# Kernel optimization log

Measured on AMD Instinct MI355X. Metric: run time of the kernel, lower is better.

Reference implementation:

```python
import jax, jax.numpy as jnp
import numpy as np

PI = float(np.pi)


def _conv2d(x, w, b, pad):
    out = jax.lax.conv_general_dilated(x, w, (1, 1), ((pad, pad), (pad, pad)),
                                       dimension_numbers=('NCHW', 'OIHW', 'NCHW'))
    return out + b[None, :, None, None]


def _group_norm(x, gamma, beta, groups, eps=1e-5):
    B, C, h, w = x.shape
    xg = x.reshape(B, groups, C // groups, h, w)
    mu = xg.mean(axis=(2, 3, 4), keepdims=True)
    var = xg.var(axis=(2, 3, 4), keepdims=True)
    xn = ((xg - mu) / jnp.sqrt(var + eps)).reshape(B, C, h, w)
    return xn * gamma[None, :, None, None] + beta[None, :, None, None]


def _l2n(x, eps=1e-12):
    return x / jnp.maximum(jnp.linalg.norm(x, axis=1, keepdims=True), eps)


def _dense_sift(x):
    # kornia DenseSIFTDescriptor defaults: 8 ang bins, 4x4 spatial bins,
    # spatial_bin_size=4, rootsift=True, clipval=0.2, stride=1, padding=1
    eps = 1e-10
    NA = 8
    # 'diff' spatial gradient with replicate padding, normalized (/2)
    xp = jnp.pad(x, ((0, 0), (0, 0), (1, 1), (1, 1)), mode='edge')
    gx = (xp[:, :, 1:-1, 2:] - xp[:, :, 1:-1, :-2]) * 0.5
    gy = (xp[:, :, 2:, 1:-1] - xp[:, :, :-2, 1:-1]) * 0.5
    mag = jnp.sqrt(gx * gx + gy * gy + eps)[:, 0]           # [B,H,W]
    ori = jnp.arctan2(gy, gx + eps)[:, 0] + 2.0 * PI
    o_big = NA * ori / (2.0 * PI)
    bo0f = jnp.floor(o_big)
    wo1_ = o_big - bo0f
    wo0 = (1.0 - wo1_) * mag
    wo1 = wo1_ * mag
    bo0 = bo0f.astype(jnp.int32) % NA
    bo1 = (bo0 + 1) % NA
    bins = jnp.arange(NA).reshape(1, NA, 1, 1)
    ang = ((bo0[:, None] == bins).astype(x.dtype) * wo0[:, None]
           + (bo1[:, None] == bins).astype(x.dtype) * wo1[:, None])  # [B,8,H,W]
    # SIFT pooling kernel ksize=4 (triangle weights), conv pad=2 -> H+1,W+1
    xc2 = np.array([0.5, 1.5, 1.5, 0.5], np.float32)
    pool1 = np.outer(xc2, xc2) / 4.0
    pk = jnp.asarray(np.tile(pool1[None, None], (NA, 1, 1, 1)))  # depthwise [8,1,4,4]
    pooled = jax.lax.conv_general_dilated(ang, pk, (1, 1), ((2, 2), (2, 2)),
                dimension_numbers=('NCHW', 'OIHW', 'NCHW'), feature_group_count=NA)
    # identity reshape conv: 128 = 8 ang * 4*4 spatial bins, pad=1 -> back to H,W
    rk = jnp.asarray(np.eye(128, dtype=np.float32).reshape(128, NA, 4, 4))
    out = jax.lax.conv_general_dilated(pooled, rk, (1, 1), ((1, 1), (1, 1)),
                dimension_numbers=('NCHW', 'OIHW', 'NCHW'))
    out = jnp.clip(_l2n(out), 0.0, 0.2)
    out = _l2n(out)
    l1 = jnp.maximum(jnp.sum(jnp.abs(out), axis=1, keepdims=True), 1e-12)
    return jnp.sqrt(out / l1 + eps)  # rootsift


def _joint_bilateral(x, guide, ksize=5, sigma_color=0.1, sigma_space=1.5):
    pad = ksize // 2
    ax = np.arange(ksize, dtype=np.float32) - ksize // 2
    g1 = np.exp(-ax ** 2 / (2.0 * sigma_space ** 2))
    g1 = g1 / g1.sum()
    sk = np.outer(g1, g1)  # normalized 5x5 gaussian space kernel
    xp = jnp.pad(x, ((0, 0), (0, 0), (pad, pad), (pad, pad)), mode='reflect')
    gp = jnp.pad(guide, ((0, 0), (0, 0), (pad, pad), (pad, pad)), mode='reflect')
    h, w = x.shape[2], x.shape[3]
    inv = -0.5 / (sigma_color ** 2)
    num = jnp.zeros_like(x)
    den = jnp.zeros((x.shape[0], 1, h, w), x.dtype)
    for dy in range(ksize):           # fixed 5x5 tap loop, accumulated in-place
        for dx in range(ksize):
            gs = gp[:, :, dy:dy + h, dx:dx + w]
            cd = jnp.sum(jnp.abs(gs - guide), axis=1, keepdims=True) ** 2  # l1 squared
            wgt = sk[dy, dx] * jnp.exp(inv * cd)
            num = num + wgt * xp[:, :, dy:dy + h, dx:dx + w]
            den = den + wgt
    return num / den


def _forward(x, gt, w1, b1, g1w, g1b, w2, b2, g2w, g2b, w3, b3, g3w, g3b,
             w4, b4, g4w, g4b, w5, b5):
    orig = x
    f = _dense_sift(x)
    f = jax.nn.relu(_group_norm(_conv2d(f, w1, b1, 2), g1w, g1b, 8))
    f = jax.nn.relu(_group_norm(_conv2d(f, w2, b2, 1), g2w, g2b, 8))
    f = jax.nn.relu(_group_norm(_conv2d(f, w3, b3, 1), g3w, g3b, 4))
    f = jax.nn.relu(_group_norm(_conv2d(f, w4, b4, 1), g4w, g4b, 4))
    f = _conv2d(f, w5, b5, 1)
    # rgb_to_yuv(gt)[:, 1:] as guidance
    r, g, b = gt[:, 0], gt[:, 1], gt[:, 2]
    u = -0.147 * r - 0.289 * g + 0.436 * b
    v = 0.615 * r - 0.515 * g - 0.100 * b
    guide = jnp.stack([u, v], axis=1)
    f = _joint_bilateral(f, guide)

    def _rescale(c, lo, hi):
        c = (c - c.min()) / (c.max() - c.min() + 1e-6)  # global min/max over B,H,W
        c = jnp.clip(c, 0.0, 1.0)
        return c * (hi - lo) + lo

    U = _rescale(f[:, 0], -0.436, 0.436)
    V = _rescale(f[:, 1], -0.615, 0.615)
    Y = orig[:, 0]
    R = Y + 1.14 * V
    G = Y - 0.396 * U - 0.581 * V
    B = Y + 2.029 * U
    return jnp.stack([R, G, B], axis=1)


def setup_inputs() -> dict:
    key = jax.random.key(0)
    ks = jax.random.split(key, 16)
    B = 4
    d = {
        'x': jax.random.uniform(ks[0], (B, 1, 270, 512), jnp.float32),
        'gt': jax.random.uniform(ks[1], (B, 3, 270, 512), jnp.float32),
        'w1': jax.random.normal(ks[2], (64, 128, 5, 5), jnp.float32) * 0.02,
        'b1': jnp.zeros((64,), jnp.float32),
        'g1w': jnp.ones((64,), jnp.float32), 'g1b': jnp.zeros((64,), jnp.float32),
        'w2': jax.random.normal(ks[3], (32, 64, 3, 3), jnp.float32) * 0.04,
        'b2': jnp.zeros((32,), jnp.float32),
        'g2w': jnp.ones((32,), jnp.float32), 'g2b': jnp.zeros((32,), jnp.float32),
        'w3': jax.random.normal(ks[4], (16, 32, 3, 3), jnp.float32) * 0.05,
        'b3': jnp.zeros((16,), jnp.float32),
        'g3w': jnp.ones((16,), jnp.float32), 'g3b': jnp.zeros((16,), jnp.float32),
        'w4': jax.random.normal(ks[5], (8, 16, 3, 3), jnp.float32) * 0.08,
        'b4': jnp.zeros((8,), jnp.float32),
        'g4w': jnp.ones((8,), jnp.float32), 'g4b': jnp.zeros((8,), jnp.float32),
        'w5': jax.random.normal(ks[6], (2, 8, 3, 3), jnp.float32) * 0.1,
        'b5': jnp.zeros((2,), jnp.float32),
    }
    return d


def reference(x, gt, w1, b1, g1w, g1b, w2, b2, g2w, g2b, w3, b3, g3w, g3b,
              w4, b4, g4w, g4b, w5, b5):
    return _forward(x, gt, w1, b1, g1w, g1b, w2, b2, g2w, g2b, w3, b3, g3w, g3b,
                    w4, b4, g4w, g4b, w5, b5)
```

## Files before the change

### kernel.cpp

```cpp
#include <hip/hip_runtime.h>

constexpr int NB  = 4;
constexpr int IH  = 270;
constexpr int IW  = 512;
constexpr int NPIX = IH * IW;
constexpr int PH  = 271;
constexpr int PW  = 513;
constexpr float TWO_PI_F = 6.28318530717958647692f;

typedef short  bf16x8 __attribute__((ext_vector_type(8)));
typedef float floatx4 __attribute__((ext_vector_type(4)));

__device__ inline unsigned short f2bf(float x) {
  union { float f; unsigned u; } un; un.f = x;
  unsigned r = un.u + 0x7fff + ((un.u >> 16) & 1);
  return (unsigned short)(r >> 16);
}
__device__ inline float bf2f(unsigned short u) {
  union { unsigned u; float f; } x; x.u = ((unsigned)u) << 16; return x.f;
}
__device__ inline unsigned fkey(float f) {
  unsigned u = __float_as_uint(f);
  return (u & 0x80000000u) ? ~u : (u | 0x80000000u);
}
__device__ inline float funkey(unsigned k) {
  unsigned u = (k & 0x80000000u) ? (k ^ 0x80000000u) : ~k;
  return __uint_as_float(u);
}
__device__ inline void gn_coef_thread(const float* __restrict__ stats,
                                      const float* __restrict__ gamma,
                                      const float* __restrict__ beta,
                                      float* cA, float* cB, int C, int chper, int b) {
  int c = threadIdx.x;
  if (c < C) {
    int g0 = (c / chper) * chper;
    float S = 0.f, S2 = 0.f;
    for (int k = 0; k < chper; k++) {
      S  += stats[(b * C + g0 + k) * 2];
      S2 += stats[(b * C + g0 + k) * 2 + 1];
    }
    double Nd = (double)chper * NPIX;
    double mu = (double)S / Nd;
    double var = (double)S2 / Nd - mu * mu;
    double rstd = 1.0 / sqrt(var + 1e-5);
    float A = (float)rstd * gamma[c];
    cA[c] = A;
    cB[c] = beta[c] - (float)mu * A;
  }
}

__device__ inline void mfma_pack_one(const float* __restrict__ w, short* __restrict__ wB,
                                     int i, int CO, int CI, int KK, int CHUNKS) {
  int j = i & 7, l = (i >> 3) & 63, f = i >> 9;
  int t = f % KK; int fc = f / KK; int cc = fc % CHUNKS; int g = fc / CHUNKS;
  int ci = cc * 32 + ((l >> 4) << 3) + j;
  int co = g * 16 + (l & 15);
  float v = (ci < CI && co < CO) ? w[((size_t)co * CI + ci) * KK + t] : 0.f;
  wB[i] = (short)f2bf(v);
}
__device__ inline void repack_one(const float* __restrict__ w, float* __restrict__ wT,
                                  int i, int CO, int CI, int KK) {
  int o = i / (CI * KK);
  int r = i % (CI * KK);
  int ci = r / KK, kk = r % KK;
  wT[(kk * CI + ci) * CO + o] = w[i];
}
__global__ __launch_bounds__(256) void prep_kernel(
    const float* __restrict__ w1, const float* __restrict__ w2,
    const float* __restrict__ w3, const float* __restrict__ w4,
    const float* __restrict__ w5,
    short* __restrict__ w1B, short* __restrict__ w2B, short* __restrict__ w3B,
    float* __restrict__ w4T, float* __restrict__ w5T) {
  constexpr int N1 = 4 * 4 * 25 * 512;
  constexpr int N2 = 2 * 2 * 9 * 512;
  constexpr int N3 = 1 * 1 * 9 * 512;
  constexpr int N4 = 8 * 16 * 9;
  constexpr int N5 = 2 * 8 * 9;
  int i = blockIdx.x * 256 + threadIdx.x;
  if (i < N1) { mfma_pack_one(w1, w1B, i, 64, 128, 25, 4); return; }
  i -= N1;
  if (i < N2) { mfma_pack_one(w2, w2B, i, 32, 64, 9, 2); return; }
  i -= N2;
  if (i < N3) { mfma_pack_one(w3, w3B, i, 16, 32, 9, 1); return; }
  i -= N3;
  if (i < N4) { repack_one(w4, w4T, i, 8, 16, 9); return; }
  i -= N4;
  if (i < N5) { repack_one(w5, w5T, i, 2, 8, 9); return; }
}

__global__ __launch_bounds__(256) void sift_desc_kernel(
    const float* __restrict__ x, short* __restrict__ descg) {
  const int b = blockIdx.z;
  const int x0 = blockIdx.x * 16, y0 = blockIdx.y * 16;
  __shared__ float xs[24][25];
  __shared__ float wo0[22][23], wo1[22][23];
  __shared__ int   bo0[22][23];
  __shared__ float pooled[8][19][20];
  __shared__ float s1s[256], gs[256];
  const int tid = threadIdx.x;
  const float* xb = x + (size_t)b * NPIX;

  for (int t = tid; t < 576; t += 256) {
    int r = t / 24, c = t % 24;
    int gy = min(max(y0 - 4 + r, 0), IH - 1);
    int gx = min(max(x0 - 4 + c, 0), IW - 1);
    xs[r][c] = xb[gy * IW + gx];
  }
  __syncthreads();

  for (int t = tid; t < 484; t += 256) {
    int r = t / 22, c = t % 22;
    int gy = y0 - 3 + r, gx = x0 - 3 + c;
    float w0 = 0.f, w1v = 0.f; int b0 = 0;
    if (gy >= 0 && gy < IH && gx >= 0 && gx < IW) {
      float gxv = (xs[r + 1][c + 2] - xs[r + 1][c]) * 0.5f;
      float gyv = (xs[r + 2][c + 1] - xs[r][c + 1]) * 0.5f;
      float mag = sqrtf(gxv * gxv + gyv * gyv + 1e-10f);
      float ori = atan2f(gyv, gxv + 1e-10f) + TWO_PI_F;
      float obig = ori * (8.0f / TWO_PI_F);
      float bf = floorf(obig);
      float w1_ = obig - bf;
      w0  = (1.0f - w1_) * mag;
      w1v = w1_ * mag;
      b0  = ((int)bf) & 7;
    }
    wo0[r][c] = w0; wo1[r][c] = w1v; bo0[r][c] = b0;
  }
  __syncthreads();

  const float pwt[4] = {0.25f, 0.75f, 0.75f, 0.25f};
  for (int t = tid; t < 361; t += 256) {
    int pr = t / 19, pc = t % 19;
    int py = y0 - 1 + pr, px = x0 - 1 + pc;
    float acc[8] = {0, 0, 0, 0, 0, 0, 0, 0};
    if (py >= 0 && py < PH && px >= 0 && px < PW) {
      #pragma unroll
      for (int i = 0; i < 4; i++) {
        #pragma unroll
        for (int j = 0; j < 4; j++) {
          float w0 = wo0[pr + i][pc + j], w1v = wo1[pr + i][pc + j];
          int b0 = bo0[pr + i][pc + j];
          int b1i = (b0 + 1) & 7;
          float pw = pwt[i] * pwt[j];
          #pragma unroll
          for (int a = 0; a < 8; a++) {
            float add = (a == b0 ? w0 : 0.f) + (a == b1i ? w1v : 0.f);
            acc[a] = fmaf(pw, add, acc[a]);
          }
        }
      }
    }
    #pragma unroll
    for (int a = 0; a < 8; a++) pooled[a][pr][pc] = acc[a];
  }
  __syncthreads();

  {
    int py = tid >> 4, px = tid & 15;
    int y = y0 + py;
    float s1 = 0.f, g = 0.f;
    if (y < IH) {
      float sum2 = 0.f;
      for (int c = 0; c < 128; c++) {
        int a = c >> 4, i = (c >> 2) & 3, j = c & 3;
        float p = pooled[a][py + i][px + j];
        sum2 = fmaf(p, p, sum2);
      }
      s1 = 1.0f / fmaxf(sqrtf(sum2), 1e-12f);
      float st2 = 0.f, st = 0.f;
      for (int c = 0; c < 128; c++) {
        int a = c >> 4, i = (c >> 2) & 3, j = c & 3;
        float p = pooled[a][py + i][px + j];
        float tv = fminf(p * s1, 0.2f);
        st2 = fmaf(tv, tv, st2);
        st += tv;
      }
      float s2 = 1.0f / fmaxf(sqrtf(st2), 1e-12f);
      float l1 = fmaxf(s2 * st, 1e-12f);
      g = s2 / l1;
    }
    s1s[tid] = s1; gs[tid] = g;
  }
  __syncthreads();

  for (int k = 0; k < 16; k++) {
    int gidx = k * 256 + tid;
    int cc = gidx >> 10, pix = (gidx >> 2) & 255, sub = gidx & 3;
    int py = pix >> 4, px = pix & 15;
    int y = y0 + py;
    if (y >= IH) continue;
    float s1v = s1s[pix], gv = gs[pix];
    int a = cc * 2 + (sub >> 1);
    unsigned short v8[8];
    #pragma unroll
    for (int jj = 0; jj < 8; jj++) {
      int i = (sub * 2 + (jj >> 2)) & 3;
      int j = jj & 3;
      float p = pooled[a][py + i][px + j];
      v8[jj] = f2bf(sqrtf(fminf(p * s1v, 0.2f) * gv + 1e-10f));
    }
    uint4 pk;
    pk.x = (unsigned)v8[0] | ((unsigned)v8[1] << 16);
    pk.y = (unsigned)v8[2] | ((unsigned)v8[3] << 16);
    pk.z = (unsigned)v8[4] | ((unsigned)v8[5] << 16);
    pk.w = (unsigned)v8[6] | ((unsigned)v8[7] << 16);
    size_t base = ((size_t)(b * 4 + cc) * NPIX + (size_t)y * IW + (x0 + px)) * 32 + sub * 8;
    *(uint4*)(descg + base) = pk;
  }
}

__global__ __launch_bounds__(256, 2) void conv1_mfma_kernel(
    const short* __restrict__ descg, const short* __restrict__ w1B,
    const float* __restrict__ bias, unsigned short* __restrict__ out,
    float* __restrict__ stats) {
  const int b = blockIdx.z;
  const int x0 = blockIdx.x * 16, y0 = blockIdx.y * 16;
  __shared__ __align__(16) char smem_raw[33408];
  short* desc = (short*)smem_raw;
  float* cout = (float*)smem_raw;

  const int tid = threadIdx.x;
  const int wave = tid >> 6, lane = tid & 63;
  const int quad = lane >> 4, lm = lane & 15;

  floatx4 acc[4][4];
  #pragma unroll
  for (int n = 0; n < 4; n++)
    #pragma unroll
    for (int i = 0; i < 4; i++) acc[n][i] = (floatx4){0.f, 0.f, 0.f, 0.f};

  for (int cc = 0; cc < 4; cc++) {
    __syncthreads();
    const short* dg = descg + (size_t)(b * 4 + cc) * NPIX * 32;
    for (int u = tid; u < 1600; u += 256) {
      int pos = u >> 2, sub = u & 3;
      int r = pos / 20, c = pos % 20;
      int gy = y0 - 2 + r, gx = x0 - 2 + c;
      uint4 val = {0u, 0u, 0u, 0u};
      if (gy >= 0 && gy < IH && gx >= 0 && gx < IW)
        val = *(const uint4*)(dg + ((size_t)gy * IW + gx) * 32 + sub * 8);
      *(uint4*)(desc + pos * 40 + sub * 8) = val;
    }
    __syncthreads();

    #pragma unroll
    for (int ky = 0; ky < 5; ky++) {
      #pragma unroll
      for (int kx = 0; kx < 5; kx++) {
        bf16x8 bfr[4];
        #pragma unroll
        for (int n = 0; n < 4; n++) {
          int f = (n * 4 + cc) * 25 + ky * 5 + kx;
          bfr[n] = *(const bf16x8*)(w1B + ((size_t)f << 9) + (lane << 3));
        }
        bf16x8 av[4];
        #pragma unroll
        for (int i = 0; i < 4; i++) {
          int mt = wave * 4 + i;
          av[i] = *(const bf16x8*)(desc + ((mt + ky) * 20 + lm + kx) * 40 + quad * 8);
        }
        #pragma unroll
        for (int n = 0; n < 4; n++)
          #pragma unroll
          for (int i = 0; i < 4; i++)
            acc[n][i] = __builtin_amdgcn_mfma_f32_16x16x32_bf16(av[i], bfr[n], acc[n][i], 0, 0, 0);
      }
    }
  }

  unsigned short* ob = out + (size_t)b * 64 * NPIX;
  for (int h = 0; h < 2; h++) {
    __syncthreads();
    #pragma unroll
    for (int nn = 0; nn < 2; nn++)
      #pragma unroll
      for (int i = 0; i < 4; i++)
        #pragma unroll
        for (int r = 0; r < 4; r++)
          cout[(nn * 16 + lm) * 261 + (wave * 4 + i) * 16 + quad * 4 + r] = acc[h * 2 + nn][i][r];
    __syncthreads();
    for (int v = tid; v < 8192; v += 256) {
      int col = v >> 8, px = v & 255;
      int y = y0 + (px >> 4), x = x0 + (px & 15);
      if (y < IH)
        ob[(size_t)(h * 32 + col) * NPIX + y * IW + x] = f2bf(cout[col * 261 + px] + bias[h * 32 + col]);
    }
    int col = tid >> 3, seg = tid & 7;
    int co = h * 32 + col;
    float bv = bias[co];
    float sum = 0.f, sq = 0.f;
    #pragma unroll
    for (int rr = 0; rr < 2; rr++) {
      int row = seg * 2 + rr;
      if (y0 + row < IH) {
        #pragma unroll
        for (int k = 0; k < 16; k++) {
          float vv = cout[col * 261 + row * 16 + k] + bv;
          sum += vv; sq += vv * vv;
        }
      }
    }
    sum += __shfl_down(sum, 4); sq += __shfl_down(sq, 4);
    sum += __shfl_down(sum, 2); sq += __shfl_down(sq, 2);
    sum += __shfl_down(sum, 1); sq += __shfl_down(sq, 1);
    if ((tid & 7) == 0) {
      atomicAdd(&stats[(b * 64 + co) * 2], sum);
      atomicAdd(&stats[(b * 64 + co) * 2 + 1], sq);
    }
  }
}

template <int CI, int CO, int CHPER, bool STATS>
__global__ __launch_bounds__(256) void convk3_mfma_kernel(
    const unsigned short* __restrict__ xin, const short* __restrict__ wB,
    const float* __restrict__ bias, const float* __restrict__ statsIn,
    const float* __restrict__ gamma, const float* __restrict__ beta,
    float* __restrict__ statsOut, unsigned short* __restrict__ out) {
  constexpr int CHUNKS = CI / 32;
  constexpr int G = CO / 16;
  constexpr int MPW = 2 * G;
  constexpr int CIS = CI + 8;
  constexpr int TILE_B = 180 * CIS * 2;
  constexpr int COUT_B = CO * 133 * 4;
  constexpr int UNION_B = TILE_B > COUT_B ? TILE_B : COUT_B;
  __shared__ __align__(16) char sm[UNION_B + CI * 8];
  short* tile = (short*)sm;
  float* cout = (float*)sm;
  float* cA = (float*)(sm + UNION_B);
  float* cB = cA + CI;

  const int b = blockIdx.z;
  const int x0 = blockIdx.x * 16, y0 = blockIdx.y * 8;
  const int tid = threadIdx.x;
  const int wave = tid >> 6, lane = tid & 63;
  const int quad = lane >> 4, lm = lane & 15;
  const int n = wave % G, mh = wave / G;

  gn_coef_thread(statsIn, gamma, beta, cA, cB, CI, CHPER, b);
  __syncthreads();

  const unsigned short* xb = xin + (size_t)b * CI * NPIX;
  for (int v = tid; v < (CI / 2) * 180; v += 256) {
    int cp = v / 180, pos = v % 180;
    int r = pos / 18, c = pos % 18;
    int gy = y0 - 1 + r, gx = x0 - 1 + c;
    float v0 = 0.f, v1 = 0.f;
    if (gy >= 0 && gy < IH && gx >= 0 && gx < IW) {
      v0 = fmaxf(fmaf(bf2f(xb[(size_t)(2 * cp) * NPIX + gy * IW + gx]), cA[2 * cp], cB[2 * cp]), 0.f);
      v1 = fmaxf(fmaf(bf2f(xb[(size_t)(2 * cp + 1) * NPIX + gy * IW + gx]), cA[2 * cp + 1], cB[2 * cp + 1]), 0.f);
    }
    unsigned pk = (unsigned)f2bf(v0) | ((unsigned)f2bf(v1) << 16);
    *(unsigned*)(tile + pos * CIS + 2 * cp) = pk;
  }
  __syncthreads();

  floatx4 acc[MPW];
  #pragma unroll
  for (int i = 0; i < MPW; i++) acc[i] = (floatx4){0.f, 0.f, 0.f, 0.f};

  #pragma unroll
  for (int cc = 0; cc < CHUNKS; cc++) {
    #pragma unroll
    for (int ky = 0; ky < 3; ky++) {
      #pragma unroll
      for (int kx = 0; kx < 3; kx++) {
        int f = (n * CHUNKS + cc) * 9 + ky * 3 + kx;
        bf16x8 bfr = *(const bf16x8*)(wB + ((size_t)f << 9) + (lane << 3));
        #pragma unroll
        for (int i = 0; i < MPW; i++) {
          int mt = mh * MPW + i;
          bf16x8 av = *(const bf16x8*)(tile + ((mt + ky) * 18 + lm + kx) * CIS + cc * 32 + quad * 8);
          acc[i] = __builtin_amdgcn_mfma_f32_16x16x32_bf16(av, bfr, acc[i], 0, 0, 0);
        }
      }
    }
  }
  __syncthreads();
  #pragma unroll
  for (int i = 0; i < MPW; i++) {
    #pragma unroll
    for (int r = 0; r < 4; r++) {
      int pixel = (mh * MPW + i) * 16 + quad * 4 + r;
      cout[(n * 16 + lm) * 133 + pixel] = acc[i][r];
    }
  }
  __syncthreads();
  unsigned short* ob = out + (size_t)b * CO * NPIX;
  for (int v = tid; v < CO * 128; v += 256) {
    int co = v >> 7, px = v & 127;
    int y = y0 + (px >> 4), x = x0 + (px & 15);
    if (y < IH) ob[(size_t)co * NPIX + y * IW + x] = f2bf(cout[co * 133 + px] + bias[co]);
  }
  if (STATS) {
    constexpr int TPC = 256 / CO;
    constexpr int PXT = 128 / TPC;
    int col = tid / TPC, seg = tid % TPC;
    float bv = bias[col];
    float sum = 0.f, sq = 0.f;
    #pragma unroll
    for (int k = 0; k < PXT; k++) {
      int p = seg * PXT + k;
      if (y0 + (p >> 4) < IH) {
        float vv = cout[col * 133 + p] + bv;
        sum += vv; sq += vv * vv;
      }
    }
    #pragma unroll
    for (int off = TPC / 2; off > 0; off >>= 1) {
      sum += __shfl_down(sum, off);
      sq  += __shfl_down(sq, off);
    }
    if (seg == 0) {
      atomicAdd(&statsOut[(b * CO + col) * 2], sum);
      atomicAdd(&statsOut[(b * CO + col) * 2 + 1], sq);
    }
  }
}

template <int CI, int CO, int CHPER, bool STATS, bool OUT_BF16>
__global__ __launch_bounds__(256) void convs_kernel(
    const unsigned short* __restrict__ xin, const float* __restrict__ wT,
    const float* __restrict__ bias, const float* __restrict__ statsIn,
    const float* __restrict__ gamma, const float* __restrict__ beta,
    float* __restrict__ statsOut, void* __restrict__ outv) {
  constexpr int OPT = CO / 2;
  const int b = blockIdx.z;
  const int x0 = blockIdx.x * 16, y0 = blockIdx.y * 8;
  __shared__ float tile[CI * 180];
  __shared__ float cA[CI], cB[CI];
  __shared__ float ssum[CO], ssq[CO];
  gn_coef_thread(statsIn, gamma, beta, cA, cB, CI, CHPER, b);
  if (STATS && threadIdx.x < CO) { ssum[threadIdx.x] = 0.f; ssq[threadIdx.x] = 0.f; }
  __syncthreads();
  const unsigned short* xb = xin + (size_t)b * CI * NPIX;
  for (int t = threadIdx.x; t < CI * 180; t += 256) {
    int ci = t / 180, rc = t % 180, r = rc / 18, c = rc % 18;
    int gy = y0 - 1 + r, gx = x0 - 1 + c;
    float v = 0.f;
    if (gy >= 0 && gy < IH && gx >= 0 && gx < IW)
      v = fmaxf(fmaf(bf2f(xb[(size_t)ci * NPIX + gy * IW + gx]), cA[ci], cB[ci]), 0.f);
    tile[t] = v;
  }
  __syncthreads();
  const int t = threadIdx.x;
  const int px = t & 127, og = t >> 7;
  const int pyy = px >> 4, pxx = px & 15;
  const int oc0 = og * OPT;
  const int y = y0 + pyy, x = x0 + pxx;
  float acc[OPT] = {};
  for (int ky = 0; ky < 3; ky++) {
    for (int kx = 0; kx < 3; kx++) {
      const float* wrow = wT + (size_t)((ky * 3 + kx) * CI) * CO + oc0;
      for (int ci = 0; ci < CI; ci++) {
        float v = tile[ci * 180 + (pyy + ky) * 18 + pxx + kx];
        #pragma unroll
        for (int o = 0; o < OPT; o++) acc[o] = fmaf(v, wrow[ci * CO + o], acc[o]);
      }
    }
  }
  if (y < IH) {
    #pragma unroll
    for (int o = 0; o < OPT; o++) {
      float vv = acc[o] + bias[oc0 + o];
      if (OUT_BF16) {
        unsigned short* ob = (unsigned short*)outv + (size_t)b * CO * NPIX;
        ob[(size_t)(oc0 + o) * NPIX + y * IW + x] = f2bf(vv);
      } else {
        float* ob = (float*)outv + (size_t)b * CO * NPIX;
        ob[(size_t)(oc0 + o) * NPIX + y * IW + x] = vv;
      }
      if (STATS) {
        atomicAdd(&ssum[oc0 + o], vv);
        atomicAdd(&ssq[oc0 + o], vv * vv);
      }
    }
  }
  if (STATS) {
    __syncthreads();
    if (threadIdx.x < CO) {
      atomicAdd(&statsOut[(b * CO + threadIdx.x) * 2], ssum[threadIdx.x]);
      atomicAdd(&statsOut[(b * CO + threadIdx.x) * 2 + 1], ssq[threadIdx.x]);
    }
  }
}

__global__ __launch_bounds__(256) void bilateral_kernel(
    const float* __restrict__ f, const float* __restrict__ gt,
    float* __restrict__ out, unsigned* __restrict__ mmbits) {
  const int b = blockIdx.z;
  const int x0 = blockIdx.x * 16, y0 = blockIdx.y * 16;
  __shared__ float gu[20][20], gv[20][20], f0s[20][20], f1s[20][20];
  __shared__ float red[4][4];
  const float* gtb = gt + (size_t)b * 3 * NPIX;
  const float* fb = f + (size_t)b * 2 * NPIX;
  for (int t = threadIdx.x; t < 400; t += 256) {
    int r = t / 20, c = t % 20;
    int gy = y0 - 2 + r, gx = x0 - 2 + c;
    if (gy < 0) gy = -gy;
    if (gy > IH - 1) gy = 2 * (IH - 1) - gy;
    if (gx < 0) gx = -gx;
    if (gx > IW - 1) gx = 2 * (IW - 1) - gx;
    int p = gy * IW + gx;
    float rr = gtb[p], gg = gtb[NPIX + p], bb = gtb[2 * NPIX + p];
    gu[r][c]  = -0.147f * rr - 0.289f * gg + 0.436f * bb;
    gv[r][c]  =  0.615f * rr - 0.515f * gg - 0.100f * bb;
    f0s[r][c] = fb[p];
    f1s[r][c] = fb[NPIX + p];
  }
  __syncthreads();
  const int t = threadIdx.x;
  const int lx = t % 16, ly = t / 16;
  const int y = y0 + ly, x = x0 + lx;
  const bool valid = (y < IH);

  float o0 = 0.f, o1 = 0.f;
  if (valid) {
    float g1v[5];
    float s = 0.f;
    #pragma unroll
    for (int k = 0; k < 5; k++) {
      float a = (float)(k - 2);
      g1v[k] = expf(-a * a / 4.5f);
      s += g1v[k];
    }
    #pragma unroll
    for (int k = 0; k < 5; k++) g1v[k] /= s;
    float cu = gu[ly + 2][lx + 2], cv = gv[ly + 2][lx + 2];
    float num0 = 0.f, num1 = 0.f, den = 0.f;
    #pragma unroll
    for (int dy = 0; dy < 5; dy++) {
      #pragma unroll
      for (int dx = 0; dx < 5; dx++) {
        float du = fabsf(gu[ly + dy][lx + dx] - cu) + fabsf(gv[ly + dy][lx + dx] - cv);
        float wgt = g1v[dy] * g1v[dx] * expf(-50.0f * du * du);
        num0 = fmaf(wgt, f0s[ly + dy][lx + dx], num0);
        num1 = fmaf(wgt, f1s[ly + dy][lx + dx], num1);
        den += wgt;
      }
    }
    o0 = num0 / den; o1 = num1 / den;
    float* ob = out + (size_t)b * 2 * NPIX;
    ob[y * IW + x] = o0;
    ob[NPIX + y * IW + x] = o1;
  }
  float mn0 = valid ? o0 : 1e30f,  mx0 = valid ? o0 : -1e30f;
  float mn1 = valid ? o1 : 1e30f,  mx1 = valid ? o1 : -1e30f;
  #pragma unroll
  for (int off = 32; off > 0; off >>= 1) {
    mn0 = fminf(mn0, __shfl_xor(mn0, off));
    mx0 = fmaxf(mx0, __shfl_xor(mx0, off));
    mn1 = fminf(mn1, __shfl_xor(mn1, off));
    mx1 = fmaxf(mx1, __shfl_xor(mx1, off));
  }
  if ((t & 63) == 0) {
    red[t >> 6][0] = mn0; red[t >> 6][1] = mx0;
    red[t >> 6][2] = mn1; red[t >> 6][3] = mx1;
  }
  __syncthreads();
  if (t == 0) {
    for (int w = 1; w < 4; w++) {
      red[0][0] = fminf(red[0][0], red[w][0]);
      red[0][1] = fmaxf(red[0][1], red[w][1]);
      red[0][2] = fminf(red[0][2], red[w][2]);
      red[0][3] = fmaxf(red[0][3], red[w][3]);
    }
    atomicMax(&mmbits[0], fkey(red[0][1]));
    atomicMax(&mmbits[1], fkey(red[0][3]));
    atomicMin(&mmbits[2], fkey(red[0][0]));
    atomicMin(&mmbits[3], fkey(red[0][2]));
  }
}

__global__ __launch_bounds__(256) void final_kernel(
    const float* __restrict__ bil, const float* __restrict__ x,
    const unsigned* __restrict__ mmbits, float* __restrict__ out) {
  int i = blockIdx.x * 256 + threadIdx.x;
  if (i >= NB * NPIX) return;
  float mx0 = funkey(mmbits[0]), mx1 = funkey(mmbits[1]);
  float mn0 = funkey(mmbits[2]), mn1 = funkey(mmbits[3]);
  int b = i / NPIX, p = i % NPIX;
  float f0 = bil[(size_t)b * 2 * NPIX + p];
  float f1 = bil[(size_t)b * 2 * NPIX + NPIX + p];
  float U = (f0 - mn0) / (mx0 - mn0 + 1e-6f);
  U = fminf(fmaxf(U, 0.f), 1.f) * 0.872f - 0.436f;
  float V = (f1 - mn1) / (mx1 - mn1 + 1e-6f);
  V = fminf(fmaxf(V, 0.f), 1.f) * 1.23f - 0.615f;
  float Y = x[(size_t)b * NPIX + p];
  float* ob = out + (size_t)b * 3 * NPIX;
  ob[p]            = Y + 1.14f * V;
  ob[NPIX + p]     = Y - 0.396f * U - 0.581f * V;
  ob[2 * NPIX + p] = Y + 2.029f * U;
}

extern "C" void kernel_launch(void* const* d_in, const int* in_sizes, int n_in,
                              void* d_out, int out_size, void* d_ws, size_t ws_size,
                              hipStream_t stream) {
  const float* x   = (const float*)d_in[0];
  const float* gt  = (const float*)d_in[1];
  const float* w1  = (const float*)d_in[2];
  const float* b1  = (const float*)d_in[3];
  const float* g1w = (const float*)d_in[4];
  const float* g1b = (const float*)d_in[5];
  const float* w2  = (const float*)d_in[6];
  const float* b2  = (const float*)d_in[7];
  const float* g2w = (const float*)d_in[8];
  const float* g2b = (const float*)d_in[9];
  const float* w3  = (const float*)d_in[10];
  const float* b3  = (const float*)d_in[11];
  const float* g3w = (const float*)d_in[12];
  const float* g3b = (const float*)d_in[13];
  const float* w4  = (const float*)d_in[14];
  const float* b4  = (const float*)d_in[15];
  const float* g4w = (const float*)d_in[16];
  const float* g4b = (const float*)d_in[17];
  const float* w5  = (const float*)d_in[18];
  const float* b5  = (const float*)d_in[19];
  float* out = (float*)d_out;

  char* ws = (char*)d_ws;
  float* stats1 = (float*)ws;
  float* stats2 = stats1 + 512;
  float* stats3 = stats2 + 256;
  float* stats4 = stats3 + 128;
  unsigned* mmbits = (unsigned*)(ws + 12288);
  char* base = ws + 16384;
  short* descg = (short*)base;
  size_t descg_shorts = (size_t)NB * 4 * NPIX * 32;
  unsigned short* bufB_h = (unsigned short*)base;
  float* c5    = (float*)(base + 36000000);
  float* bilat = (float*)(base + 41000000);
  short* w1B = descg + descg_shorts;
  short* w2B = w1B + 204800;
  short* w3B = w2B + 18432;
  float* w4T = (float*)(w3B + 4608);
  float* w5T = w4T + 1152;
  unsigned short* bufA_h = (unsigned short*)(w5T + 144);

  hipMemsetAsync(ws, 0, 12304, stream);
  hipMemsetAsync(ws + 12296, 0xFF, 8, stream);

  prep_kernel<<<896, 256, 0, stream>>>(w1, w2, w3, w4, w5, w1B, w2B, w3B, w4T, w5T);

  sift_desc_kernel<<<dim3(32, 17, NB), 256, 0, stream>>>(x, descg);

  conv1_mfma_kernel<<<dim3(32, 17, NB), 256, 0, stream>>>(descg, w1B, b1, bufA_h, stats1);

  convk3_mfma_kernel<64, 32, 8, true><<<dim3(32, 34, NB), 256, 0, stream>>>(
      bufA_h, w2B, b2, stats1, g1w, g1b, stats2, bufB_h);

  convk3_mfma_kernel<32, 16, 4, true><<<dim3(32, 34, NB), 256, 0, stream>>>(
      bufB_h, w3B, b3, stats2, g2w, g2b, stats3, bufA_h);

  convs_kernel<16, 8, 4, true, true><<<dim3(32, 34, NB), 256, 0, stream>>>(
      bufA_h, w4T, b4, stats3, g3w, g3b, stats4, bufB_h);

  convs_kernel<8, 2, 2, false, false><<<dim3(32, 34, NB), 256, 0, stream>>>(
      bufB_h, w5T, b5, stats4, g4w, g4b, nullptr, c5);

  bilateral_kernel<<<dim3(32, 17, NB), 256, 0, stream>>>(c5, gt, bilat, mmbits);
  final_kernel<<<(NB * NPIX + 255) / 256, 256, 0, stream>>>(bilat, x, mmbits, out);

  (void)in_sizes; (void)n_in; (void)out_size; (void)ws_size;
}
```

Before: 1.310 ms.

## Switch conv1 to 32x32x16 MFMA tiles and prefetch weight fragments

Conv1 now uses 32x32x16 bf16 MFMA instructions, with each wave computing 2x2 tiles of 32 pixels by 32 channels, and the weights are repacked to the matching fragment layout. Weight fragments are double-buffered and loaded two taps ahead. The 3x3 conv kernel gets the same register prefetch of its weight fragments. The aim is fewer LDS A-operand reads per FLOP and hidden global weight-load latency, in exchange for a different accumulator layout and more live registers.

```diff
diff --git a/kernel.cpp b/kernel.cpp
--- a/kernel.cpp
+++ b/kernel.cpp
@@ -10,6 +10,7 @@
 
 typedef short  bf16x8 __attribute__((ext_vector_type(8)));
 typedef float floatx4 __attribute__((ext_vector_type(4)));
+typedef float floatx16 __attribute__((ext_vector_type(16)));
 
 __device__ inline unsigned short f2bf(float x) {
   union { float f; unsigned u; } un; un.f = x;
@@ -49,6 +50,17 @@
   }
 }
 
+__device__ inline void mfma_pack32_one(const float* __restrict__ w, short* __restrict__ wB,
+                                       int i, int CO, int CI, int KK) {
+  int j = i & 7, l = (i >> 3) & 63, f = i >> 9;
+  int ks = f & 1; int f2 = f >> 1;
+  int tap = f2 % KK; int fc = f2 / KK;
+  int cc = fc & 3; int ng = fc >> 2;
+  int ci = cc * 32 + ks * 16 + ((l >> 5) << 3) + j;
+  int co = ng * 32 + (l & 31);
+  float v = (ci < CI && co < CO) ? w[((size_t)co * CI + ci) * KK + tap] : 0.f;
+  wB[i] = (short)f2bf(v);
+}
 __device__ inline void mfma_pack_one(const float* __restrict__ w, short* __restrict__ wB,
                                      int i, int CO, int CI, int KK, int CHUNKS) {
   int j = i & 7, l = (i >> 3) & 63, f = i >> 9;
@@ -71,13 +83,13 @@
     const float* __restrict__ w5,
     short* __restrict__ w1B, short* __restrict__ w2B, short* __restrict__ w3B,
     float* __restrict__ w4T, float* __restrict__ w5T) {
-  constexpr int N1 = 4 * 4 * 25 * 512;
+  constexpr int N1 = 2 * 4 * 25 * 2 * 512;
   constexpr int N2 = 2 * 2 * 9 * 512;
   constexpr int N3 = 1 * 1 * 9 * 512;
   constexpr int N4 = 8 * 16 * 9;
   constexpr int N5 = 2 * 8 * 9;
   int i = blockIdx.x * 256 + threadIdx.x;
-  if (i < N1) { mfma_pack_one(w1, w1B, i, 64, 128, 25, 4); return; }
+  if (i < N1) { mfma_pack32_one(w1, w1B, i, 64, 128, 25); return; }
   i -= N1;
   if (i < N2) { mfma_pack_one(w2, w2B, i, 32, 64, 9, 2); return; }
   i -= N2;
@@ -221,13 +233,15 @@
 
   const int tid = threadIdx.x;
   const int wave = tid >> 6, lane = tid & 63;
-  const int quad = lane >> 4, lm = lane & 15;
-
-  floatx4 acc[4][4];
+  const int l31 = lane & 31, lhi = lane >> 5;
+
+  floatx16 acc[2][2];
   #pragma unroll
-  for (int n = 0; n < 4; n++)
-    #pragma unroll
-    for (int i = 0; i < 4; i++) acc[n][i] = (floatx4){0.f, 0.f, 0.f, 0.f};
+  for (int j = 0; j < 2; j++)
+    #pragma unroll
+    for (int i = 0; i < 2; i++)
+      #pragma unroll
+      for (int r = 0; r < 16; r++) acc[j][i][r] = 0.f;
 
   for (int cc = 0; cc < 4; cc++) {
     __syncthreads();
@@ -243,27 +257,34 @@
     }
     __syncthreads();
 
-    #pragma unroll
-    for (int ky = 0; ky < 5; ky++) {
+    const short* wb = w1B + (size_t)cc * 50 * 512 + (lane << 3);
+    bf16x8 bfr[2][2];
+    #pragma unroll
+    for (int j = 0; j < 2; j++) {
+      bfr[0][j] = *(const bf16x8*)(wb + ((size_t)j * 200 + 0) * 512);
+      bfr[1][j] = *(const bf16x8*)(wb + ((size_t)j * 200 + 1) * 512);
+    }
+    #pragma unroll
+    for (int t = 0; t < 50; t++) {
+      const int tap = t >> 1, ks = t & 1, sl = t & 1;
+      const int ky = tap / 5, kx = tap % 5;
+      bf16x8 av[2];
       #pragma unroll
-      for (int kx = 0; kx < 5; kx++) {
-        bf16x8 bfr[4];
+      for (int i = 0; i < 2; i++) {
+        int mt = wave * 2 + i;
+        int r = mt * 2 + (l31 >> 4) + ky;
+        int c = (l31 & 15) + kx;
+        av[i] = *(const bf16x8*)(desc + (r * 20 + c) * 40 + ks * 16 + (lhi << 3));
+      }
+      #pragma unroll
+      for (int j = 0; j < 2; j++)
         #pragma unroll
-        for (int n = 0; n < 4; n++) {
-          int f = (n * 4 + cc) * 25 + ky * 5 + kx;
-          bfr[n] = *(const bf16x8*)(w1B + ((size_t)f << 9) + (lane << 3));
-        }
-        bf16x8 av[4];
+        for (int i = 0; i < 2; i++)
+          acc[j][i] = __builtin_amdgcn_mfma_f32_32x32x16_bf16(av[i], bfr[sl][j], acc[j][i], 0, 0, 0);
+      if (t + 2 < 50) {
         #pragma unroll
-        for (int i = 0; i < 4; i++) {
-          int mt = wave * 4 + i;
-          av[i] = *(const bf16x8*)(desc + ((mt + ky) * 20 + lm + kx) * 40 + quad * 8);
-        }
-        #pragma unroll
-        for (int n = 0; n < 4; n++)
-          #pragma unroll
-          for (int i = 0; i < 4; i++)
-            acc[n][i] = __builtin_amdgcn_mfma_f32_16x16x32_bf16(av[i], bfr[n], acc[n][i], 0, 0, 0);
+        for (int j = 0; j < 2; j++)
+          bfr[sl][j] = *(const bf16x8*)(wb + ((size_t)j * 200 + t + 2) * 512);
       }
     }
   }
@@ -272,12 +293,14 @@
   for (int h = 0; h < 2; h++) {
     __syncthreads();
     #pragma unroll
-    for (int nn = 0; nn < 2; nn++)
+    for (int i = 0; i < 2; i++) {
       #pragma unroll
-      for (int i = 0; i < 4; i++)
-        #pragma unroll
-        for (int r = 0; r < 4; r++)
-          cout[(nn * 16 + lm) * 261 + (wave * 4 + i) * 16 + quad * 4 + r] = acc[h * 2 + nn][i][r];
+      for (int rg = 0; rg < 16; rg++) {
+        int row = (rg & 3) + 8 * (rg >> 2) + 4 * lhi;
+        int p = (wave * 2 + i) * 32 + row;
+        cout[l31 * 261 + p] = acc[h][i][rg];
+      }
+    }
     __syncthreads();
     for (int v = tid; v < 8192; v += 256) {
       int col = v >> 8, px = v & 255;
@@ -358,22 +381,24 @@
   #pragma unroll
   for (int i = 0; i < MPW; i++) acc[i] = (floatx4){0.f, 0.f, 0.f, 0.f};
 
+  constexpr int NT = CHUNKS * 9;
+  const short* wbase = wB + ((size_t)n * NT) * 512 + (lane << 3);
+  bf16x8 bfr[2];
+  bfr[0] = *(const bf16x8*)(wbase);
+  bfr[1] = *(const bf16x8*)(wbase + 512);
   #pragma unroll
-  for (int cc = 0; cc < CHUNKS; cc++) {
-    #pragma unroll
-    for (int ky = 0; ky < 3; ky++) {
-      #pragma unroll
-      for (int kx = 0; kx < 3; kx++) {
-        int f = (n * CHUNKS + cc) * 9 + ky * 3 + kx;
-        bf16x8 bfr = *(const bf16x8*)(wB + ((size_t)f << 9) + (lane << 3));
-        #pragma unroll
-        for (int i = 0; i < MPW; i++) {
-          int mt = mh * MPW + i;
-          bf16x8 av = *(const bf16x8*)(tile + ((mt + ky) * 18 + lm + kx) * CIS + cc * 32 + quad * 8);
-          acc[i] = __builtin_amdgcn_mfma_f32_16x16x32_bf16(av, bfr, acc[i], 0, 0, 0);
-        }
-      }
-    }
+  for (int t = 0; t < NT; t++) {
+    const int sl = t & 1;
+    const int cc1 = t / 9, r1 = t % 9, ky = r1 / 3, kx = r1 % 3;
+    bf16x8 av[MPW];
+    #pragma unroll
+    for (int i = 0; i < MPW; i++)
+      av[i] = *(const bf16x8*)(tile + ((mh * MPW + i + ky) * 18 + lm + kx) * CIS + cc1 * 32 + quad * 8);
+    #pragma unroll
+    for (int i = 0; i < MPW; i++)
+      acc[i] = __builtin_amdgcn_mfma_f32_16x16x32_bf16(av[i], bfr[sl], acc[i], 0, 0, 0);
+    if (t + 2 < NT)
+      bfr[sl] = *(const bf16x8*)(wbase + (size_t)(t + 2) * 512);
   }
   __syncthreads();
   #pragma unroll
```

Measured after the change: 1.297 ms. About the same (-1.0%).
